# Optimization experiments

Measured on AMD Instinct MI355X. Metric: run time of the kernel, lower is better.

The kernel has to match this reference:

```python
import jax, jax.numpy as jnp
import numpy as np

EPS = 1e-6
HEAD_DIM = 64
N_Q = 16
N_KV = 2

def setup_inputs() -> dict:
    key = jax.random.key(0)
    ks = jax.random.split(key, 4)
    H = 1024
    x = jax.random.normal(ks[0], (4, 8192, H), dtype=jnp.float32)
    ln_weight = jnp.zeros((H,), dtype=jnp.float32)  # Gemma param; scale is (1 + w)
    wq = jax.random.normal(ks[1], (H, HEAD_DIM * N_Q), dtype=jnp.float32) / np.sqrt(H)
    wk = jax.random.normal(ks[2], (H, HEAD_DIM * N_KV), dtype=jnp.float32) / np.sqrt(H)
    wv = jax.random.normal(ks[3], (H, HEAD_DIM * N_KV), dtype=jnp.float32) / np.sqrt(H)
    return {"x": x, "ln_weight": ln_weight, "wq": wq, "wk": wk, "wv": wv}

def gemma_rms_norm(x, w):
    xf = x.astype(jnp.float32)
    h = xf * jax.lax.rsqrt(jnp.mean(xf * xf, axis=-1, keepdims=True) + EPS)
    return (h * (1.0 + w.astype(jnp.float32))).astype(x.dtype)

def reference(x, ln_weight, wq, wk, wv):
    # Gemma RMSNorm prologue, then three linear projections (no bias).
    h = gemma_rms_norm(x, ln_weight)            # [B, S, H]
    q = jnp.einsum('bsh,hd->bsd', h, wq)        # [B, S, nq*d]
    k = jnp.einsum('bsh,hd->bsd', h, wk)        # [B, S, nkv*d]
    v = jnp.einsum('bsh,hd->bsd', h, wv)
    B, S = x.shape[0], x.shape[1]
    q = q.reshape(B, S, N_Q, HEAD_DIM)
    k = k.reshape(B, S, N_KV, HEAD_DIM)
    v = v.reshape(B, S, N_KV, HEAD_DIM)
    return (q, k, v)
```

## Files before the change

### kernel.cpp

```cpp
#include <hip/hip_runtime.h>
#include <hip/hip_bf16.h>

typedef __attribute__((ext_vector_type(4))) float f32x4;
typedef __attribute__((ext_vector_type(8))) short bf16x8;

#define H 1024
#define NTOT 1280
#define BM 128
#define BN 128
#define BK 64
#define NKT 16
#define NTILES 10

static __device__ __forceinline__ unsigned short f2bf(float f) {
    __hip_bfloat16 b = __float2bfloat16(f);
    return __builtin_bit_cast(unsigned short, b);
}

#define GLOAD_LDS16(g, l)                                                     \
    __builtin_amdgcn_global_load_lds(                                         \
        (const __attribute__((address_space(1))) void*)(g),                   \
        (__attribute__((address_space(3))) void*)(l), 16, 0, 0)

__global__ __launch_bounds__(256) void k_pre(const float* __restrict__ x,
                                             const float* __restrict__ wq,
                                             const float* __restrict__ wk,
                                             const float* __restrict__ wv,
                                             const float* __restrict__ lnw,
                                             __hip_bfloat16* __restrict__ h,
                                             __hip_bfloat16* __restrict__ Bt,
                                             int nrms) {
    __shared__ float l[64][65];
    const int t = threadIdx.x;

    if ((int)blockIdx.x < nrms) {
        const int wave = t >> 6;
        const int lane = t & 63;
        const size_t row = (size_t)blockIdx.x * 4 + wave;

        const float4* xr = (const float4*)(x + row * H);
        float4 v[4];
        float ss = 0.f;
#pragma unroll
        for (int i = 0; i < 4; ++i) {
            v[i] = xr[lane + 64 * i];
            ss += v[i].x * v[i].x + v[i].y * v[i].y + v[i].z * v[i].z + v[i].w * v[i].w;
        }
#pragma unroll
        for (int o = 1; o < 64; o <<= 1) ss += __shfl_xor(ss, o);
        const float sc = rsqrtf(ss * (1.0f / H) + 1e-6f);

        ushort4* hr = (ushort4*)(h + row * H);
#pragma unroll
        for (int i = 0; i < 4; ++i) {
            ushort4 o4;
            o4.x = f2bf(v[i].x * sc);
            o4.y = f2bf(v[i].y * sc);
            o4.z = f2bf(v[i].z * sc);
            o4.w = f2bf(v[i].w * sc);
            hr[lane + 64 * i] = o4;
        }
    } else {
        const int b = (int)blockIdx.x - nrms;
        const int kt = b & 15;
        const int ntl = b >> 4;
        const int k0 = kt * 64, n0 = ntl * 64;
        const float* src; int ldn, nb;
        if (n0 < 1024)      { src = wq; ldn = 1024; nb = n0; }
        else if (n0 < 1152) { src = wk; ldn = 128;  nb = n0 - 1024; }
        else                { src = wv; ldn = 128;  nb = n0 - 1152; }
        const int nl = t & 63, kl = t >> 6;
#pragma unroll
        for (int i = 0; i < 16; ++i) {
            const int k = kl + i * 4;
            l[k][nl] = (1.0f + lnw[k0 + k]) * src[(size_t)(k0 + k) * ldn + nb + nl];
        }
        __syncthreads();
        const int k2 = t & 63, n2 = t >> 6;
#pragma unroll
        for (int i = 0; i < 16; ++i) {
            const int n = n2 + i * 4;
            Bt[(size_t)(n0 + n) * 1024 + k0 + k2] = __float2bfloat16(l[k2][n]);
        }
    }
}

__global__ __launch_bounds__(256, 2) void k_gemm(const __hip_bfloat16* __restrict__ A,
                                                 const __hip_bfloat16* __restrict__ Bt,
                                                 float* __restrict__ out, int rows) {
    __shared__ __align__(16) char smem[65536];

    const int tid = threadIdx.x;
    const int lane = tid & 63;
    const int wid = tid >> 6;
    const int wm = wid >> 1;
    const int wn = wid & 1;

    const int cpx = gridDim.x >> 3;
    const int wg = (blockIdx.x & 7) * cpx + (blockIdx.x >> 3);
    const int nt = wg % NTILES;
    const int mt = wg / NTILES;
    const size_t m0 = (size_t)mt * BM;

    const int r = tid >> 3;
    const int cswz = ((tid & 7) * 16) ^ ((r & 7) << 4);
    const char* aG = (const char*)A + (m0 + r) * (size_t)(H * 2) + cswz;
    const char* bG = (const char*)Bt + ((size_t)nt * BN + r) * (size_t)(H * 2) + cswz;

#define STAGE(buf, kt)                                                        \
    {                                                                         \
        _Pragma("unroll") for (int q = 0; q < 4; ++q)                         \
            GLOAD_LDS16(aG + (size_t)(kt) * 128 + (size_t)q * 32 * (H * 2),   \
                        smem + (buf) * 32768 + q * 4096 + tid * 16);          \
        _Pragma("unroll") for (int q = 0; q < 4; ++q)                         \
            GLOAD_LDS16(bG + (size_t)(kt) * 128 + (size_t)q * 32 * (H * 2),   \
                        smem + (buf) * 32768 + 16384 + q * 4096 + tid * 16);  \
    }

    const int rowA = wm * 64 + (lane & 15);
    const int rowB = wn * 64 + (lane & 15);
    const int xm = (lane & 7) << 4;
    const int c0 = (((lane >> 4) * 16)) ^ xm;
    const int c1 = (64 + ((lane >> 4) * 16)) ^ xm;

    f32x4 acc[4][4] = {};

#define TILE(cur, kt, DS, VM)                                                 \
    {                                                                         \
        const char* aL = smem + (cur) * 32768;                                \
        const char* bL = aL + 16384;                                          \
        asm volatile("s_waitcnt vmcnt(" VM ")" ::: "memory");                 \
        __builtin_amdgcn_s_barrier();                                         \
        __builtin_amdgcn_sched_barrier(0);                                    \
        bf16x8 a0[4], b0[4];                                                  \
        _Pragma("unroll") for (int mi = 0; mi < 4; ++mi)                      \
            a0[mi] = *(const bf16x8*)(aL + (rowA + mi * 16) * 128 + c0);      \
        _Pragma("unroll") for (int ni = 0; ni < 4; ++ni)                      \
            b0[ni] = *(const bf16x8*)(bL + (rowB + ni * 16) * 128 + c0);      \
        bf16x8 a1[4], b1[4];                                                  \
        _Pragma("unroll") for (int mi = 0; mi < 4; ++mi)                      \
            a1[mi] = *(const bf16x8*)(aL + (rowA + mi * 16) * 128 + c1);      \
        _Pragma("unroll") for (int ni = 0; ni < 4; ++ni)                      \
            b1[ni] = *(const bf16x8*)(bL + (rowB + ni * 16) * 128 + c1);      \
        __builtin_amdgcn_s_setprio(1);                                        \
        _Pragma("unroll") for (int mi = 0; mi < 4; ++mi)                      \
            _Pragma("unroll") for (int ni = 0; ni < 4; ++ni)                  \
                acc[mi][ni] = __builtin_amdgcn_mfma_f32_16x16x32_bf16(        \
                    a0[mi], b0[ni], acc[mi][ni], 0, 0, 0);                    \
        __builtin_amdgcn_s_setprio(0);                                        \
        asm volatile("s_waitcnt lgkmcnt(0)" ::: "memory");                    \
        __builtin_amdgcn_sched_barrier(0);                \
        __builtin_amdgcn_s_barrier();                                         \
        __builtin_amdgcn_sched_barrier(0);                                    \
        if (DS) STAGE(cur, (kt) + 2);                                         \
        __builtin_amdgcn_s_setprio(1);                                        \
        _Pragma("unroll") for (int mi = 0; mi < 4; ++mi)                      \
            _Pragma("unroll") for (int ni = 0; ni < 4; ++ni)                  \
                acc[mi][ni] = __builtin_amdgcn_mfma_f32_16x16x32_bf16(        \
                    a1[mi], b1[ni], acc[mi][ni], 0, 0, 0);                    \
        __builtin_amdgcn_s_setprio(0);                                        \
    }

    STAGE(0, 0);
    STAGE(1, 1);

    for (int kt = 0; kt < NKT - 4; kt += 2) {
        TILE(0, kt, 1, "8");
        TILE(1, kt + 1, 1, "8");
    }
    TILE(0, NKT - 4, 1, "8");
    TILE(1, NKT - 3, 1, "8");
    TILE(0, NKT - 2, 0, "8");
    TILE(1, NKT - 1, 0, "0");

    const size_t QSZ = (size_t)rows * 1024;
    const size_t KSZ = (size_t)rows * 128;
    const int colg0 = nt * BN + wn * 64;
    float* op;
    int ldc, cb0;
    if (colg0 < 1024)      { op = out;             ldc = 1024; cb0 = colg0; }
    else if (colg0 < 1152) { op = out + QSZ;       ldc = 128;  cb0 = colg0 - 1024; }
    else                   { op = out + QSZ + KSZ; ldc = 128;  cb0 = colg0 - 1152; }

    const size_t r0 = m0 + wm * 64 + ((lane >> 4) * 4);
    const int cc0 = cb0 + (lane & 15);
#pragma unroll
    for (int mi = 0; mi < 4; ++mi)
#pragma unroll
        for (int ni = 0; ni < 4; ++ni)
#pragma unroll
            for (int rr = 0; rr < 4; ++rr)
                op[(r0 + mi * 16 + rr) * (size_t)ldc + cc0 + ni * 16] = acc[mi][ni][rr];
}

extern "C" void kernel_launch(void* const* d_in, const int* in_sizes, int n_in,
                              void* d_out, int out_size, void* d_ws, size_t ws_size,
                              hipStream_t stream) {
    const float* x   = (const float*)d_in[0];
    const float* lnw = (const float*)d_in[1];
    const float* wq  = (const float*)d_in[2];
    const float* wk  = (const float*)d_in[3];
    const float* wv  = (const float*)d_in[4];
    float* out = (float*)d_out;

    const int rows = in_sizes[0] / H;

    __hip_bfloat16* Bt = (__hip_bfloat16*)d_ws;
    __hip_bfloat16* h  = (__hip_bfloat16*)((char*)d_ws + (size_t)NTOT * H * 2);

    const int nrms = rows / 4;
    k_pre<<<nrms + 320, 256, 0, stream>>>(x, wq, wk, wv, lnw, h, Bt, nrms);
    k_gemm<<<(rows / BM) * NTILES, 256, 0, stream>>>(h, Bt, out, rows);
}
```

Before: 135.5 us.

## Switch GEMM mainloop to BK=32 triple-buffered LDS pipeline with one barrier per step

```diff
diff --git a/kernel.cpp b/kernel.cpp
--- a/kernel.cpp
+++ b/kernel.cpp
@@ -8,8 +8,8 @@
 #define NTOT 1280
 #define BM 128
 #define BN 128
-#define BK 64
-#define NKT 16
+#define BK 32
+#define NST 32
 #define NTILES 10
 
 static __device__ __forceinline__ unsigned short f2bf(float f) {
@@ -88,7 +88,7 @@
 __global__ __launch_bounds__(256, 2) void k_gemm(const __hip_bfloat16* __restrict__ A,
                                                  const __hip_bfloat16* __restrict__ Bt,
                                                  float* __restrict__ out, int rows) {
-    __shared__ __align__(16) char smem[65536];
+    __shared__ __align__(16) char smem[49152];
 
     const int tid = threadIdx.x;
     const int lane = tid & 63;
@@ -102,76 +102,65 @@
     const int mt = wg / NTILES;
     const size_t m0 = (size_t)mt * BM;
 
-    const int r = tid >> 3;
-    const int cswz = ((tid & 7) * 16) ^ ((r & 7) << 4);
-    const char* aG = (const char*)A + (m0 + r) * (size_t)(H * 2) + cswz;
-    const char* bG = (const char*)Bt + ((size_t)nt * BN + r) * (size_t)(H * 2) + cswz;
+    const char* aSrc[2];
+    const char* bSrc[2];
+#pragma unroll
+    for (int j = 0; j < 2; ++j) {
+        const int d = tid + j * 256;
+        const int rp = d >> 3, s = (d & 7) ^ (rp & 7);
+        const int row = rp * 2 + (s >> 2), kg = s & 3;
+        aSrc[j] = (const char*)A + (m0 + row) * (size_t)(H * 2) + kg * 16;
+        bSrc[j] = (const char*)Bt + ((size_t)nt * BN + row) * (size_t)(H * 2) + kg * 16;
+    }
 
 #define STAGE(buf, kt)                                                        \
     {                                                                         \
-        _Pragma("unroll") for (int q = 0; q < 4; ++q)                         \
-            GLOAD_LDS16(aG + (size_t)(kt) * 128 + (size_t)q * 32 * (H * 2),   \
-                        smem + (buf) * 32768 + q * 4096 + tid * 16);          \
-        _Pragma("unroll") for (int q = 0; q < 4; ++q)                         \
-            GLOAD_LDS16(bG + (size_t)(kt) * 128 + (size_t)q * 32 * (H * 2),   \
-                        smem + (buf) * 32768 + 16384 + q * 4096 + tid * 16);  \
-    }
-
-    const int rowA = wm * 64 + (lane & 15);
-    const int rowB = wn * 64 + (lane & 15);
-    const int xm = (lane & 7) << 4;
-    const int c0 = (((lane >> 4) * 16)) ^ xm;
-    const int c1 = (64 + ((lane >> 4) * 16)) ^ xm;
+        _Pragma("unroll") for (int j = 0; j < 2; ++j)                         \
+            GLOAD_LDS16(aSrc[j] + (size_t)(kt) * 64,                          \
+                        smem + (buf) * 16384 + (tid + j * 256) * 16);         \
+        _Pragma("unroll") for (int j = 0; j < 2; ++j)                         \
+            GLOAD_LDS16(bSrc[j] + (size_t)(kt) * 64,                          \
+                        smem + (buf) * 16384 + 8192 + (tid + j * 256) * 16);  \
+    }
+
+    const int fb = ((lane & 15) >> 1) * 128
+                 + (((((lane & 1) << 2) + (lane >> 4)) ^ ((lane & 15) >> 1)) << 4);
 
     f32x4 acc[4][4] = {};
 
-#define TILE(cur, kt, DS, VM)                                                 \
+#define STEP(buf, sbuf, kt, DS, VM)                                           \
     {                                                                         \
-        const char* aL = smem + (cur) * 32768;                                \
-        const char* bL = aL + 16384;                                          \
+        const char* aL = smem + (buf) * 16384;                                \
+        const char* bL = aL + 8192;                                           \
         asm volatile("s_waitcnt vmcnt(" VM ")" ::: "memory");                 \
         __builtin_amdgcn_s_barrier();                                         \
         __builtin_amdgcn_sched_barrier(0);                                    \
-        bf16x8 a0[4], b0[4];                                                  \
+        bf16x8 af[4], bfv[4];                                                 \
         _Pragma("unroll") for (int mi = 0; mi < 4; ++mi)                      \
-            a0[mi] = *(const bf16x8*)(aL + (rowA + mi * 16) * 128 + c0);      \
+            af[mi] = *(const bf16x8*)(aL + fb + (wm * 4 + mi) * 1024);        \
         _Pragma("unroll") for (int ni = 0; ni < 4; ++ni)                      \
-            b0[ni] = *(const bf16x8*)(bL + (rowB + ni * 16) * 128 + c0);      \
-        bf16x8 a1[4], b1[4];                                                  \
-        _Pragma("unroll") for (int mi = 0; mi < 4; ++mi)                      \
-            a1[mi] = *(const bf16x8*)(aL + (rowA + mi * 16) * 128 + c1);      \
-        _Pragma("unroll") for (int ni = 0; ni < 4; ++ni)                      \
-            b1[ni] = *(const bf16x8*)(bL + (rowB + ni * 16) * 128 + c1);      \
+            bfv[ni] = *(const bf16x8*)(bL + fb + (wn * 4 + ni) * 1024);       \
+        if (DS) STAGE(sbuf, (kt) + 2);                                        \
         __builtin_amdgcn_s_setprio(1);                                        \
         _Pragma("unroll") for (int mi = 0; mi < 4; ++mi)                      \
             _Pragma("unroll") for (int ni = 0; ni < 4; ++ni)                  \
                 acc[mi][ni] = __builtin_amdgcn_mfma_f32_16x16x32_bf16(        \
-                    a0[mi], b0[ni], acc[mi][ni], 0, 0, 0);                    \
+                    af[mi], bfv[ni], acc[mi][ni], 0, 0, 0);                   \
         __builtin_amdgcn_s_setprio(0);                                        \
         asm volatile("s_waitcnt lgkmcnt(0)" ::: "memory");                    \
-        __builtin_amdgcn_sched_barrier(0);                \
-        __builtin_amdgcn_s_barrier();                                         \
-        __builtin_amdgcn_sched_barrier(0);                                    \
-        if (DS) STAGE(cur, (kt) + 2);                                         \
-        __builtin_amdgcn_s_setprio(1);                                        \
-        _Pragma("unroll") for (int mi = 0; mi < 4; ++mi)                      \
-            _Pragma("unroll") for (int ni = 0; ni < 4; ++ni)                  \
-                acc[mi][ni] = __builtin_amdgcn_mfma_f32_16x16x32_bf16(        \
-                    a1[mi], b1[ni], acc[mi][ni], 0, 0, 0);                    \
-        __builtin_amdgcn_s_setprio(0);                                        \
+        __builtin_amdgcn_sched_barrier(0);    \
     }
 
     STAGE(0, 0);
     STAGE(1, 1);
 
-    for (int kt = 0; kt < NKT - 4; kt += 2) {
-        TILE(0, kt, 1, "8");
-        TILE(1, kt + 1, 1, "8");
-    }
-    TILE(0, NKT - 4, 1, "8");
-    TILE(1, NKT - 3, 1, "8");
-    TILE(0, NKT - 2, 0, "8");
-    TILE(1, NKT - 1, 0, "0");
+    for (int kt = 0; kt < 30; kt += 3) {
+        STEP(0, 2, kt, 1, "4");
+        STEP(1, 0, kt + 1, 1, "4");
+        STEP(2, 1, kt + 2, 1, "4");
+    }
+    STEP(0, 2, 30, 0, "4");
+    STEP(1, 0, 31, 0, "0");
 
     const size_t QSZ = (size_t)rows * 1024;
     const size_t KSZ = (size_t)rows * 128;
```

Result: slower. 149.9 us (+10.7%).
